# Performance work log

Hardware: AMD Instinct MI355X
Metric: run time of the kernel (lower is better)

## Reference

```python
import jax, jax.numpy as jnp
import numpy as np

# Sizes (see shape_source)
N_P, N_C, E = 65536, 8192, 131072
D_P, D_C, D_ADD, D_EDGE, D_HID = 80, 48, 16, 8, 64
F_IN = D_P + D_C + D_ADD  # 144, message_input_irreps dim


def setup_inputs() -> dict:
    key = jax.random.key(0)
    ks = jax.random.split(key, 8)
    x_p = jax.random.normal(ks[0], (N_P, D_P), jnp.float32)
    x_c = jax.random.normal(ks[1], (N_C, D_C), jnp.float32)
    src = jax.random.randint(ks[2], (E,), 0, N_C)  # indexes x_c (edge_index[0])
    dst = jax.random.randint(ks[3], (E,), 0, N_P)  # indexes x_p (edge_index[1])
    edge_index = jnp.stack([src, dst], axis=0)
    edge_attr = jax.random.normal(ks[4], (E, D_EDGE), jnp.float32)
    additional_message_features = jax.random.normal(ks[5], (E, D_ADD), jnp.float32)
    batch = jnp.zeros((N_P,), jnp.int32)  # single graph; unused when norm=None
    # Fully-connected tensor-product weights (scalar irreps -> bilinear map) + scalar bias
    W1 = jax.random.normal(ks[6], (F_IN, D_EDGE, D_HID), jnp.float32) / np.float32(np.sqrt(F_IN * D_EDGE))
    b1 = jnp.zeros((D_HID,), jnp.float32)
    W2 = jax.random.normal(ks[7], (D_HID, D_EDGE, D_HID), jnp.float32) / np.float32(np.sqrt(D_HID * D_EDGE))
    b2 = jnp.zeros((D_HID,), jnp.float32)
    return {"x_p": x_p, "x_c": x_c, "edge_index": edge_index, "edge_attr": edge_attr,
            "batch": batch, "additional_message_features": additional_message_features,
            "W1": W1, "b1": b1, "W2": W2, "b2": b2}


def _tp(x, a, W, b):
    """Fully-connected O3 tensor product on scalar irreps: out[e,h] = sum_{f,g} x[e,f] a[e,g] W[f,g,h] + b[h]."""
    # contract feature axis first to avoid the [E, F, G] outer product
    y = (x @ W.reshape(W.shape[0], -1)).reshape(x.shape[0], a.shape[1], -1)  # [E, G, H]
    return jnp.einsum('eg,egh->eh', a, y) + b


def reference(x_p, x_c, edge_index, edge_attr, batch, additional_message_features, W1, b1, W2, b2):
    src, dst = edge_index[0], edge_index[1]
    # gather: [E, D_P + D_C + D_ADD]
    inp = jnp.concatenate([x_p[dst], x_c[src], additional_message_features], axis=-1)
    # two O3TensorProductSwishGate message layers (scalar irreps -> bilinear + swish)
    m = jax.nn.silu(_tp(inp, edge_attr, W1, b1))
    m = jax.nn.silu(_tp(m, edge_attr, W2, b2))
    # scatter-sum over destination (particle) nodes, then concat with residual features
    agg = jax.ops.segment_sum(m, dst, num_segments=x_p.shape[0])
    return jnp.concatenate([x_p, agg], axis=-1)  # [N_P, D_P + D_HID]
```

## Files before the change

kernel.cpp:

```cpp
#include <hip/hip_runtime.h>
#include <hip/hip_bf16.h>

#define E_CNT 131072
#define NP_CNT 65536
#define NC_CNT 8192
#define D_P 80
#define D_C 48
#define D_ADD 16
#define D_HID 64
#define K1 1152
#define K2 512

typedef short bf16x8 __attribute__((ext_vector_type(8)));
typedef float f32x4 __attribute__((ext_vector_type(4)));

__device__ __forceinline__ unsigned short f2bf(float x){
  unsigned u = __builtin_bit_cast(unsigned, x);
  u = u + 0x7FFFu + ((u >> 16) & 1u);
  return (unsigned short)(u >> 16);
}
__device__ __forceinline__ float bf2f(unsigned short b){
  unsigned u = ((unsigned)b) << 16;
  return __builtin_bit_cast(float, u);
}
__device__ __forceinline__ unsigned pk2(float a, float b){
  return (unsigned)f2bf(a) | ((unsigned)f2bf(b) << 16);
}
__device__ __forceinline__ float silu_f(float x){
  return x / (1.0f + __expf(-x));
}

__global__ void prep_w_kernel(const float* __restrict__ W1, const float* __restrict__ W2,
                              unsigned short* __restrict__ wt1, unsigned short* __restrict__ wt2){
  int id = blockIdx.x * 256 + threadIdx.x;
  if (id < 64 * K1){
    int h = id / K1;
    int k = id - h * K1;
    wt1[id] = f2bf(W1[k * 64 + h]);
  } else {
    int id2 = id - 64 * K1;
    int h = id2 / K2;
    int k = id2 - h * K2;
    wt2[id2] = f2bf(W2[k * 64 + h]);
  }
}

__global__ void init_out_kernel(const float4* __restrict__ xp4, float4* __restrict__ out4){
  int i4 = blockIdx.x * 256 + threadIdx.x;
  int row = i4 / 36;
  int jq = i4 - row * 36;
  float4 z = make_float4(0.f, 0.f, 0.f, 0.f);
  out4[i4] = (jq < 20) ? xp4[row * 20 + jq] : z;
}

template<int KTOT, bool SECOND>
__global__ __launch_bounds__(256) void msg_gemm_kernel(
    const float* __restrict__ x_p, const float* __restrict__ x_c,
    const int* __restrict__ eidx, const float* __restrict__ ea,
    const float* __restrict__ addf,
    const unsigned short* __restrict__ wt, const float* __restrict__ bias,
    const unsigned short* __restrict__ m1in,
    unsigned short* __restrict__ m1out,
    float* __restrict__ out)
{
  __shared__ unsigned int s_xa[256 * 32];
  __shared__ unsigned int s_w [64 * 32];
  __shared__ int s_dst[256];

  const int t    = threadIdx.x;
  const int e    = blockIdx.x * 256 + t;
  const int lane = t & 63;
  const int wv   = t >> 6;
  const int l15  = lane & 15;
  const int q    = lane >> 4;

  float af[8];
  {
    const float4* ap = reinterpret_cast<const float4*>(ea + (size_t)e * 8);
    float4 a0 = ap[0], a1 = ap[1];
    af[0] = a0.x; af[1] = a0.y; af[2] = a0.z; af[3] = a0.w;
    af[4] = a1.x; af[5] = a1.y; af[6] = a1.z; af[7] = a1.w;
  }
  const int dstI = eidx[E_CNT + e];
  int srcI = 0;
  if constexpr (!SECOND) srcI = eidx[e];
  if constexpr (SECOND)  s_dst[t] = dstI;

  f32x4 acc[4][4];
  #pragma unroll
  for (int i = 0; i < 4; ++i)
    #pragma unroll
    for (int j = 0; j < 4; ++j)
      acc[i][j] = f32x4{0.f, 0.f, 0.f, 0.f};

  constexpr int NCH = KTOT / 64;
  for (int c = 0; c < NCH; ++c){
    float xv[8];
    if constexpr (!SECOND){
      const int fb = c * 8;
      if (fb < D_P){
        const float4* p = reinterpret_cast<const float4*>(x_p + (size_t)dstI * D_P + fb);
        float4 v0 = p[0], v1 = p[1];
        xv[0]=v0.x; xv[1]=v0.y; xv[2]=v0.z; xv[3]=v0.w;
        xv[4]=v1.x; xv[5]=v1.y; xv[6]=v1.z; xv[7]=v1.w;
      } else if (fb < D_P + D_C){
        const float4* p = reinterpret_cast<const float4*>(x_c + (size_t)srcI * D_C + (fb - D_P));
        float4 v0 = p[0], v1 = p[1];
        xv[0]=v0.x; xv[1]=v0.y; xv[2]=v0.z; xv[3]=v0.w;
        xv[4]=v1.x; xv[5]=v1.y; xv[6]=v1.z; xv[7]=v1.w;
      } else {
        const float4* p = reinterpret_cast<const float4*>(addf + (size_t)e * D_ADD + (fb - D_P - D_C));
        float4 v0 = p[0], v1 = p[1];
        xv[0]=v0.x; xv[1]=v0.y; xv[2]=v0.z; xv[3]=v0.w;
        xv[4]=v1.x; xv[5]=v1.y; xv[6]=v1.z; xv[7]=v1.w;
      }
    } else {
      const uint4 mv = *reinterpret_cast<const uint4*>(m1in + (size_t)e * 64 + c * 8);
      const unsigned short* ms = reinterpret_cast<const unsigned short*>(&mv);
      #pragma unroll
      for (int fl = 0; fl < 8; ++fl) xv[fl] = bf2f(ms[fl]);
    }
    #pragma unroll
    for (int fl = 0; fl < 8; ++fl){
      float x = xv[fl];
      uint4 wv4;
      wv4.x = pk2(x * af[0], x * af[1]);
      wv4.y = pk2(x * af[2], x * af[3]);
      wv4.z = pk2(x * af[4], x * af[5]);
      wv4.w = pk2(x * af[6], x * af[7]);
      const int slot = fl ^ (t & 7);
      *reinterpret_cast<uint4*>(&s_xa[t * 32 + slot * 4]) = wv4;
    }
    {
      const int h = t >> 2, part = t & 3;
      const unsigned short* gw = wt + (size_t)h * KTOT + c * 64;
      #pragma unroll
      for (int qq = 0; qq < 2; ++qq){
        const int sl = part * 2 + qq;
        uint4 v = *reinterpret_cast<const uint4*>(gw + sl * 8);
        const int phys = sl ^ (h & 7);
        *reinterpret_cast<uint4*>(&s_w[h * 32 + phys * 4]) = v;
      }
    }
    __syncthreads();
    #pragma unroll
    for (int ks = 0; ks < 2; ++ks){
      bf16x8 Af[4], Bf[4];
      #pragma unroll
      for (int mt = 0; mt < 4; ++mt){
        const int er = wv * 64 + mt * 16 + l15;
        const int slot = (ks * 4 + q) ^ (er & 7);
        Af[mt] = __builtin_bit_cast(bf16x8, *reinterpret_cast<const uint4*>(&s_xa[er * 32 + slot * 4]));
      }
      #pragma unroll
      for (int nt = 0; nt < 4; ++nt){
        const int hr = nt * 16 + l15;
        const int slot = (ks * 4 + q) ^ (hr & 7);
        Bf[nt] = __builtin_bit_cast(bf16x8, *reinterpret_cast<const uint4*>(&s_w[hr * 32 + slot * 4]));
      }
      #pragma unroll
      for (int mt = 0; mt < 4; ++mt)
        #pragma unroll
        for (int nt = 0; nt < 4; ++nt)
          acc[mt][nt] = __builtin_amdgcn_mfma_f32_16x16x32_bf16(Af[mt], Bf[nt], acc[mt][nt], 0, 0, 0);
    }
    __syncthreads();
  }

  float bv[4];
  #pragma unroll
  for (int nt = 0; nt < 4; ++nt) bv[nt] = bias[nt * 16 + l15];

  #pragma unroll
  for (int mt = 0; mt < 4; ++mt){
    #pragma unroll
    for (int nt = 0; nt < 4; ++nt){
      #pragma unroll
      for (int r = 0; r < 4; ++r){
        float x = acc[mt][nt][r] + bv[nt];
        float s = silu_f(x);
        const int er = wv * 64 + mt * 16 + q * 4 + r;
        if constexpr (!SECOND){
          m1out[(size_t)(blockIdx.x * 256 + er) * 64 + nt * 16 + l15] = f2bf(s);
        } else {
          unsafeAtomicAdd(out + (size_t)s_dst[er] * 144 + 80 + nt * 16 + l15, s);
        }
      }
    }
  }
}

extern "C" void kernel_launch(void* const* d_in, const int* in_sizes, int n_in,
                              void* d_out, int out_size, void* d_ws, size_t ws_size,
                              hipStream_t stream){
  const float* x_p  = (const float*)d_in[0];
  const float* x_c  = (const float*)d_in[1];
  const int*   eidx = (const int*)d_in[2];
  const float* ea   = (const float*)d_in[3];
  const float* addf = (const float*)d_in[5];
  const float* W1   = (const float*)d_in[6];
  const float* b1   = (const float*)d_in[7];
  const float* W2   = (const float*)d_in[8];
  const float* b2   = (const float*)d_in[9];
  float* out = (float*)d_out;

  char* ws = (char*)d_ws;
  unsigned short* wt1 = (unsigned short*)(ws);
  unsigned short* wt2 = (unsigned short*)(ws + 163840);
  unsigned short* m1  = (unsigned short*)(ws + 262144);

  prep_w_kernel<<<(64 * K1 + 64 * K2) / 256, 256, 0, stream>>>(W1, W2, wt1, wt2);
  init_out_kernel<<<(NP_CNT * 36) / 256, 256, 0, stream>>>((const float4*)x_p, (float4*)out);
  msg_gemm_kernel<K1, false><<<E_CNT / 256, 256, 0, stream>>>(
      x_p, x_c, eidx, ea, addf, wt1, b1, nullptr, m1, nullptr);
  msg_gemm_kernel<K2, true><<<E_CNT / 256, 256, 0, stream>>>(
      x_p, x_c, eidx, ea, addf, wt2, b2, m1, nullptr, out);
}
```

Measured before the change: 114.3 us.

## Switch to fp16 packed outer products with 128-edge tiles and two threads per edge

Operands move from bf16 to fp16, so the edge_attr outer product can be built with packed half multiplies (cvt_pkrtz plus f16x2 mul) instead of per-element float multiply and manual bf16 rounding. Each block now covers 128 edges with two threads per edge, which halves per-thread feature loads and accumulator registers. Launch bounds request 4 blocks per CU, and the weight global loads are issued before the A-tile construction to overlap their latency. The intermediate activations are stored as fp16, which has less exponent range than bf16, and the fp16 products risk overflow or precision loss. Weight tiles are now staged twice as often per edge.

```diff
diff --git a/kernel.cpp b/kernel.cpp
--- a/kernel.cpp
+++ b/kernel.cpp
@@ -3,45 +3,36 @@
 
 #define E_CNT 131072
 #define NP_CNT 65536
-#define NC_CNT 8192
 #define D_P 80
 #define D_C 48
 #define D_ADD 16
-#define D_HID 64
 #define K1 1152
 #define K2 512
 
-typedef short bf16x8 __attribute__((ext_vector_type(8)));
+typedef _Float16 f16x8 __attribute__((ext_vector_type(8)));
+typedef _Float16 f16x4 __attribute__((ext_vector_type(4)));
+typedef _Float16 f16x2 __attribute__((ext_vector_type(2)));
 typedef float f32x4 __attribute__((ext_vector_type(4)));
 
-__device__ __forceinline__ unsigned short f2bf(float x){
-  unsigned u = __builtin_bit_cast(unsigned, x);
-  u = u + 0x7FFFu + ((u >> 16) & 1u);
-  return (unsigned short)(u >> 16);
-}
-__device__ __forceinline__ float bf2f(unsigned short b){
-  unsigned u = ((unsigned)b) << 16;
-  return __builtin_bit_cast(float, u);
-}
-__device__ __forceinline__ unsigned pk2(float a, float b){
-  return (unsigned)f2bf(a) | ((unsigned)f2bf(b) << 16);
-}
 __device__ __forceinline__ float silu_f(float x){
   return x / (1.0f + __expf(-x));
 }
+__device__ __forceinline__ f16x2 pkrtz(float a, float b){
+  return __builtin_bit_cast(f16x2, __builtin_amdgcn_cvt_pkrtz(a, b));
+}
 
 __global__ void prep_w_kernel(const float* __restrict__ W1, const float* __restrict__ W2,
-                              unsigned short* __restrict__ wt1, unsigned short* __restrict__ wt2){
+                              _Float16* __restrict__ wt1, _Float16* __restrict__ wt2){
   int id = blockIdx.x * 256 + threadIdx.x;
   if (id < 64 * K1){
     int h = id / K1;
     int k = id - h * K1;
-    wt1[id] = f2bf(W1[k * 64 + h]);
+    wt1[id] = (_Float16)W1[k * 64 + h];
   } else {
     int id2 = id - 64 * K1;
     int h = id2 / K2;
     int k = id2 - h * K2;
-    wt2[id2] = f2bf(W2[k * 64 + h]);
+    wt2[id2] = (_Float16)W2[k * 64 + h];
   }
 }
 
@@ -54,115 +45,118 @@
 }
 
 template<int KTOT, bool SECOND>
-__global__ __launch_bounds__(256) void msg_gemm_kernel(
+__global__ __launch_bounds__(256, 4) void msg_gemm_kernel(
     const float* __restrict__ x_p, const float* __restrict__ x_c,
     const int* __restrict__ eidx, const float* __restrict__ ea,
     const float* __restrict__ addf,
-    const unsigned short* __restrict__ wt, const float* __restrict__ bias,
-    const unsigned short* __restrict__ m1in,
-    unsigned short* __restrict__ m1out,
+    const _Float16* __restrict__ wt, const float* __restrict__ bias,
+    const _Float16* __restrict__ m1in,
+    _Float16* __restrict__ m1out,
     float* __restrict__ out)
 {
-  __shared__ unsigned int s_xa[256 * 32];
+  __shared__ unsigned int s_xa[128 * 32];
   __shared__ unsigned int s_w [64 * 32];
-  __shared__ int s_dst[256];
+  __shared__ int s_dst[128];
 
   const int t    = threadIdx.x;
-  const int e    = blockIdx.x * 256 + t;
+  const int er   = t >> 1;
+  const int hh   = t & 1;
+  const int e    = blockIdx.x * 128 + er;
   const int lane = t & 63;
   const int wv   = t >> 6;
   const int l15  = lane & 15;
   const int q    = lane >> 4;
 
-  float af[8];
+  f16x2 apk[4];
   {
     const float4* ap = reinterpret_cast<const float4*>(ea + (size_t)e * 8);
     float4 a0 = ap[0], a1 = ap[1];
-    af[0] = a0.x; af[1] = a0.y; af[2] = a0.z; af[3] = a0.w;
-    af[4] = a1.x; af[5] = a1.y; af[6] = a1.z; af[7] = a1.w;
+    apk[0] = pkrtz(a0.x, a0.y);
+    apk[1] = pkrtz(a0.z, a0.w);
+    apk[2] = pkrtz(a1.x, a1.y);
+    apk[3] = pkrtz(a1.z, a1.w);
   }
   const int dstI = eidx[E_CNT + e];
   int srcI = 0;
   if constexpr (!SECOND) srcI = eidx[e];
-  if constexpr (SECOND)  s_dst[t] = dstI;
-
-  f32x4 acc[4][4];
+  if constexpr (SECOND)  s_dst[er] = dstI;
+
+  f32x4 acc[2][4];
   #pragma unroll
-  for (int i = 0; i < 4; ++i)
+  for (int i = 0; i < 2; ++i)
     #pragma unroll
     for (int j = 0; j < 4; ++j)
       acc[i][j] = f32x4{0.f, 0.f, 0.f, 0.f};
 
   constexpr int NCH = KTOT / 64;
   for (int c = 0; c < NCH; ++c){
-    float xv[8];
+    uint4 wreg[2];
+    const int wh = t >> 2, wpart = t & 3;
+    {
+      const _Float16* gw = wt + (size_t)wh * KTOT + c * 64;
+      #pragma unroll
+      for (int qq = 0; qq < 2; ++qq)
+        wreg[qq] = *reinterpret_cast<const uint4*>(gw + (wpart * 2 + qq) * 8);
+    }
+    f16x2 xbc[4];
     if constexpr (!SECOND){
-      const int fb = c * 8;
-      if (fb < D_P){
-        const float4* p = reinterpret_cast<const float4*>(x_p + (size_t)dstI * D_P + fb);
-        float4 v0 = p[0], v1 = p[1];
-        xv[0]=v0.x; xv[1]=v0.y; xv[2]=v0.z; xv[3]=v0.w;
-        xv[4]=v1.x; xv[5]=v1.y; xv[6]=v1.z; xv[7]=v1.w;
-      } else if (fb < D_P + D_C){
-        const float4* p = reinterpret_cast<const float4*>(x_c + (size_t)srcI * D_C + (fb - D_P));
-        float4 v0 = p[0], v1 = p[1];
-        xv[0]=v0.x; xv[1]=v0.y; xv[2]=v0.z; xv[3]=v0.w;
-        xv[4]=v1.x; xv[5]=v1.y; xv[6]=v1.z; xv[7]=v1.w;
-      } else {
-        const float4* p = reinterpret_cast<const float4*>(addf + (size_t)e * D_ADD + (fb - D_P - D_C));
-        float4 v0 = p[0], v1 = p[1];
-        xv[0]=v0.x; xv[1]=v0.y; xv[2]=v0.z; xv[3]=v0.w;
-        xv[4]=v1.x; xv[5]=v1.y; xv[6]=v1.z; xv[7]=v1.w;
-      }
+      const int fb = c * 8 + hh * 4;
+      const float* src;
+      if (fb < D_P)            src = x_p  + (size_t)dstI * D_P   + fb;
+      else if (fb < D_P + D_C) src = x_c  + (size_t)srcI * D_C   + (fb - D_P);
+      else                     src = addf + (size_t)e    * D_ADD + (fb - D_P - D_C);
+      float4 v = *reinterpret_cast<const float4*>(src);
+      xbc[0] = pkrtz(v.x, v.x);
+      xbc[1] = pkrtz(v.y, v.y);
+      xbc[2] = pkrtz(v.z, v.z);
+      xbc[3] = pkrtz(v.w, v.w);
     } else {
-      const uint4 mv = *reinterpret_cast<const uint4*>(m1in + (size_t)e * 64 + c * 8);
-      const unsigned short* ms = reinterpret_cast<const unsigned short*>(&mv);
-      #pragma unroll
-      for (int fl = 0; fl < 8; ++fl) xv[fl] = bf2f(ms[fl]);
-    }
-    #pragma unroll
-    for (int fl = 0; fl < 8; ++fl){
-      float x = xv[fl];
-      uint4 wv4;
-      wv4.x = pk2(x * af[0], x * af[1]);
-      wv4.y = pk2(x * af[2], x * af[3]);
-      wv4.z = pk2(x * af[4], x * af[5]);
-      wv4.w = pk2(x * af[6], x * af[7]);
-      const int slot = fl ^ (t & 7);
-      *reinterpret_cast<uint4*>(&s_xa[t * 32 + slot * 4]) = wv4;
-    }
-    {
-      const int h = t >> 2, part = t & 3;
-      const unsigned short* gw = wt + (size_t)h * KTOT + c * 64;
-      #pragma unroll
-      for (int qq = 0; qq < 2; ++qq){
-        const int sl = part * 2 + qq;
-        uint4 v = *reinterpret_cast<const uint4*>(gw + sl * 8);
-        const int phys = sl ^ (h & 7);
-        *reinterpret_cast<uint4*>(&s_w[h * 32 + phys * 4]) = v;
-      }
+      const _Float16* mp = m1in + (size_t)e * 64 + c * 8 + hh * 4;
+      f16x4 mh = __builtin_bit_cast(f16x4, *reinterpret_cast<const uint2*>(mp));
+      #pragma unroll
+      for (int j = 0; j < 4; ++j){ xbc[j] = f16x2{mh[j], mh[j]}; }
+    }
+    #pragma unroll
+    for (int fl = 0; fl < 4; ++fl){
+      f16x2 p0 = xbc[fl] * apk[0];
+      f16x2 p1 = xbc[fl] * apk[1];
+      f16x2 p2 = xbc[fl] * apk[2];
+      f16x2 p3 = xbc[fl] * apk[3];
+      uint4 w4;
+      w4.x = __builtin_bit_cast(unsigned, p0);
+      w4.y = __builtin_bit_cast(unsigned, p1);
+      w4.z = __builtin_bit_cast(unsigned, p2);
+      w4.w = __builtin_bit_cast(unsigned, p3);
+      const int slot = (hh * 4 + fl) ^ (er & 7);
+      *reinterpret_cast<uint4*>(&s_xa[er * 32 + slot * 4]) = w4;
+    }
+    #pragma unroll
+    for (int qq = 0; qq < 2; ++qq){
+      const int sl = wpart * 2 + qq;
+      const int phys = sl ^ (wh & 7);
+      *reinterpret_cast<uint4*>(&s_w[wh * 32 + phys * 4]) = wreg[qq];
     }
     __syncthreads();
     #pragma unroll
     for (int ks = 0; ks < 2; ++ks){
-      bf16x8 Af[4], Bf[4];
-      #pragma unroll
-      for (int mt = 0; mt < 4; ++mt){
-        const int er = wv * 64 + mt * 16 + l15;
-        const int slot = (ks * 4 + q) ^ (er & 7);
-        Af[mt] = __builtin_bit_cast(bf16x8, *reinterpret_cast<const uint4*>(&s_xa[er * 32 + slot * 4]));
+      f16x8 Af[2], Bf[4];
+      #pragma unroll
+      for (int mt = 0; mt < 2; ++mt){
+        const int erow = wv * 32 + mt * 16 + l15;
+        const int slot = (ks * 4 + q) ^ (erow & 7);
+        Af[mt] = __builtin_bit_cast(f16x8, *reinterpret_cast<const uint4*>(&s_xa[erow * 32 + slot * 4]));
       }
       #pragma unroll
       for (int nt = 0; nt < 4; ++nt){
         const int hr = nt * 16 + l15;
         const int slot = (ks * 4 + q) ^ (hr & 7);
-        Bf[nt] = __builtin_bit_cast(bf16x8, *reinterpret_cast<const uint4*>(&s_w[hr * 32 + slot * 4]));
+        Bf[nt] = __builtin_bit_cast(f16x8, *reinterpret_cast<const uint4*>(&s_w[hr * 32 + slot * 4]));
       }
       #pragma unroll
-      for (int mt = 0; mt < 4; ++mt)
+      for (int mt = 0; mt < 2; ++mt)
         #pragma unroll
         for (int nt = 0; nt < 4; ++nt)
-          acc[mt][nt] = __builtin_amdgcn_mfma_f32_16x16x32_bf16(Af[mt], Bf[nt], acc[mt][nt], 0, 0, 0);
+          acc[mt][nt] = __builtin_amdgcn_mfma_f32_16x16x32_f16(Af[mt], Bf[nt], acc[mt][nt], 0, 0, 0);
     }
     __syncthreads();
   }
@@ -172,18 +166,18 @@
   for (int nt = 0; nt < 4; ++nt) bv[nt] = bias[nt * 16 + l15];
 
   #pragma unroll
-  for (int mt = 0; mt < 4; ++mt){
+  for (int mt = 0; mt < 2; ++mt){
     #pragma unroll
     for (int nt = 0; nt < 4; ++nt){
       #pragma unroll
       for (int r = 0; r < 4; ++r){
         float x = acc[mt][nt][r] + bv[nt];
         float s = silu_f(x);
-        const int er = wv * 64 + mt * 16 + q * 4 + r;
+        const int erow = wv * 32 + mt * 16 + q * 4 + r;
         if constexpr (!SECOND){
-          m1out[(size_t)(blockIdx.x * 256 + er) * 64 + nt * 16 + l15] = f2bf(s);
+          m1out[(size_t)(blockIdx.x * 128 + erow) * 64 + nt * 16 + l15] = (_Float16)s;
         } else {
-          unsafeAtomicAdd(out + (size_t)s_dst[er] * 144 + 80 + nt * 16 + l15, s);
+          unsafeAtomicAdd(out + (size_t)s_dst[erow] * 144 + 80 + nt * 16 + l15, s);
         }
       }
     }
@@ -205,14 +199,14 @@
   float* out = (float*)d_out;
 
   char* ws = (char*)d_ws;
-  unsigned short* wt1 = (unsigned short*)(ws);
-  unsigned short* wt2 = (unsigned short*)(ws + 163840);
-  unsigned short* m1  = (unsigned short*)(ws + 262144);
+  _Float16* wt1 = (_Float16*)(ws);
+  _Float16* wt2 = (_Float16*)(ws + 163840);
+  _Float16* m1  = (_Float16*)(ws + 262144);
 
   prep_w_kernel<<<(64 * K1 + 64 * K2) / 256, 256, 0, stream>>>(W1, W2, wt1, wt2);
   init_out_kernel<<<(NP_CNT * 36) / 256, 256, 0, stream>>>((const float4*)x_p, (float4*)out);
-  msg_gemm_kernel<K1, false><<<E_CNT / 256, 256, 0, stream>>>(
+  msg_gemm_kernel<K1, false><<<E_CNT / 128, 256, 0, stream>>>(
       x_p, x_c, eidx, ea, addf, wt1, b1, nullptr, m1, nullptr);
-  msg_gemm_kernel<K2, true><<<E_CNT / 256, 256, 0, stream>>>(
+  msg_gemm_kernel<K2, true><<<E_CNT / 128, 256, 0, stream>>>(
       x_p, x_c, eidx, ea, addf, wt2, b2, m1, nullptr, out);
 }
```

Result: faster. 91.84 us (-19.7%).
